# Kernel tuning notes

Hardware: AMD Instinct MI355X
Metric: run time of the kernel (lower is better)

The kernel has to match this reference:

```python
import jax, jax.numpy as jnp
import numpy as np

N = 512
C = 64
B = 1048576


def setup_inputs() -> dict:
    key = jax.random.key(0)
    k1, k2, k3, k4 = jax.random.split(key, 4)
    coords = jax.random.uniform(k1, (B, 3), dtype=jnp.float32, minval=-0.5, maxval=0.5)
    x_line = jax.random.normal(k2, (N, C), dtype=jnp.float32)
    y_line = jax.random.normal(k3, (N, C), dtype=jnp.float32)
    z_line = jax.random.normal(k4, (N, C), dtype=jnp.float32)
    grid = jnp.linspace(-0.5, 0.5, N, dtype=jnp.float32)
    return {"coords": coords, "x_line": x_line, "y_line": y_line, "z_line": z_line, "grid": grid}


def _interp_1d(line_feat, coord, grid):
    # line_feat: [N, C], coord: [B] in [-0.5, 0.5]
    n = line_feat.shape[0]
    pos = (coord - grid[0]) / (grid[1] - grid[0])          # [B] fractional index
    idx0 = jnp.clip(jnp.floor(pos).astype(jnp.int32), 0, n - 2)
    w1 = (pos - idx0.astype(pos.dtype))[:, None]            # [B, 1]
    f0 = line_feat[idx0]                                    # [B, C] gather
    f1 = line_feat[idx0 + 1]                                # [B, C] gather
    return f0 * (1.0 - w1) + f1 * w1


def reference(coords, x_line, y_line, z_line, grid):
    # mode='sum' (default): fx + fy + fz -> [B, C]
    fx = _interp_1d(x_line, coords[:, 0], grid)
    fy = _interp_1d(y_line, coords[:, 1], grid)
    fz = _interp_1d(z_line, coords[:, 2], grid)
    return fx + fy + fz
```

## Files before the change

kernel.cpp:

```cpp
#include <hip/hip_runtime.h>


typedef float f4 __attribute__((ext_vector_type(4)));

constexpr int kN  = 512;
constexpr int kC4 = 16;

__global__ __launch_bounds__(256) void triline_kernel(
    const float* __restrict__ coords,
    const f4* __restrict__ xl,
    const f4* __restrict__ yl,
    const f4* __restrict__ zl,
    const float* __restrict__ grid,
    f4* __restrict__ out,
    int total)
{
    int gid = blockIdx.x * 256 + threadIdx.x;
    if (gid >= total) return;
    int b  = gid >> 4;
    int c4 = gid & 15;

    float g0     = grid[0];
    float inv_dg = 1.0f / (grid[1] - g0);

    float cx = coords[3 * b + 0];
    float cy = coords[3 * b + 1];
    float cz = coords[3 * b + 2];

    float px = (cx - g0) * inv_dg;
    float py = (cy - g0) * inv_dg;
    float pz = (cz - g0) * inv_dg;

    int ix = min(max((int)floorf(px), 0), kN - 2);
    int iy = min(max((int)floorf(py), 0), kN - 2);
    int iz = min(max((int)floorf(pz), 0), kN - 2);

    float wx = px - (float)ix;
    float wy = py - (float)iy;
    float wz = pz - (float)iz;

    f4 x0 = xl[ix * kC4 + c4];
    f4 x1 = xl[ix * kC4 + kC4 + c4];
    f4 y0 = yl[iy * kC4 + c4];
    f4 y1 = yl[iy * kC4 + kC4 + c4];
    f4 z0 = zl[iz * kC4 + c4];
    f4 z1 = zl[iz * kC4 + kC4 + c4];

    f4 r = x0 + (x1 - x0) * wx;
    r    = r + y0 + (y1 - y0) * wy;
    r    = r + z0 + (z1 - z0) * wz;

    __builtin_nontemporal_store(r, &out[gid]);
}

extern "C" void kernel_launch(void* const* d_in, const int* in_sizes, int n_in,
                              void* d_out, int out_size, void* d_ws, size_t ws_size,
                              hipStream_t stream) {
    const float* coords = (const float*)d_in[0];
    const f4*    xl     = (const f4*)d_in[1];
    const f4*    yl     = (const f4*)d_in[2];
    const f4*    zl     = (const f4*)d_in[3];
    const float* grid   = (const float*)d_in[4];
    f4*          out    = (f4*)d_out;

    int B      = in_sizes[0] / 3;
    int total  = B * kC4;
    int blocks = (total + 255) / 256;

    triline_kernel<<<blocks, 256, 0, stream>>>(coords, xl, yl, zl, grid, out, total);
}
```

Before: 332.9 us.

## Stage channel-group slices of line tables in LDS as bf16 with persistent blocks

```diff
diff --git a/kernel.cpp b/kernel.cpp
--- a/kernel.cpp
+++ b/kernel.cpp
@@ -2,55 +2,110 @@
 
 
 typedef float f4 __attribute__((ext_vector_type(4)));
+typedef unsigned short u16;
+typedef u16 us4 __attribute__((ext_vector_type(4)));
 
-constexpr int kN  = 512;
-constexpr int kC4 = 16;
+constexpr int kN        = 512;
+constexpr int kC4       = 16;
+constexpr int kGroups   = 4;
+constexpr int kStride   = 20;
+constexpr int kParts    = 128;
+constexpr int kThreads  = 1024;
 
-__global__ __launch_bounds__(256) void triline_kernel(
+__device__ __forceinline__ u16 f32_to_bf16_rn(float f) {
+    unsigned int u = __builtin_bit_cast(unsigned int, f);
+    unsigned int r = (u + 0x7FFFu + ((u >> 16) & 1u)) >> 16;
+    return (u16)r;
+}
+__device__ __forceinline__ float bf16_to_f32(u16 h) {
+    unsigned int u = ((unsigned int)h) << 16;
+    return __builtin_bit_cast(float, u);
+}
+__device__ __forceinline__ f4 us4_to_f4(us4 h) {
+    f4 r;
+    r.x = bf16_to_f32(h.x); r.y = bf16_to_f32(h.y);
+    r.z = bf16_to_f32(h.z); r.w = bf16_to_f32(h.w);
+    return r;
+}
+
+__global__ __launch_bounds__(kThreads) void triline_kernel(
     const float* __restrict__ coords,
     const f4* __restrict__ xl,
     const f4* __restrict__ yl,
     const f4* __restrict__ zl,
     const float* __restrict__ grid,
     f4* __restrict__ out,
-    int total)
+    int B)
 {
-    int gid = blockIdx.x * 256 + threadIdx.x;
-    if (gid >= total) return;
-    int b  = gid >> 4;
-    int c4 = gid & 15;
+    __shared__ u16 s_tab[3 * kN * kStride];
+
+    const int tid   = threadIdx.x;
+    const int g     = blockIdx.x & (kGroups - 1);
+    const int part  = blockIdx.x >> 2;
+    const int pts   = B / kParts;
+    const int pbase = part * pts;
+
+    for (int s = tid; s < 3 * kN * 4; s += kThreads) {
+        int t  = s >> 11;
+        int rq = s & 2047;
+        int r  = rq >> 2;
+        int q  = rq & 3;
+        const f4* tp = (t == 0) ? xl : ((t == 1) ? yl : zl);
+        f4 v = tp[r * kC4 + g * 4 + q];
+        us4 h;
+        h.x = f32_to_bf16_rn(v.x); h.y = f32_to_bf16_rn(v.y);
+        h.z = f32_to_bf16_rn(v.z); h.w = f32_to_bf16_rn(v.w);
+        *(us4*)&s_tab[t * (kN * kStride) + r * kStride + q * 4] = h;
+    }
 
     float g0     = grid[0];
     float inv_dg = 1.0f / (grid[1] - g0);
 
-    float cx = coords[3 * b + 0];
-    float cy = coords[3 * b + 1];
-    float cz = coords[3 * b + 2];
+    __syncthreads();
 
-    float px = (cx - g0) * inv_dg;
-    float py = (cy - g0) * inv_dg;
-    float pz = (cz - g0) * inv_dg;
+    const u16* sx = &s_tab[0];
+    const u16* sy = &s_tab[kN * kStride];
+    const u16* sz = &s_tab[2 * kN * kStride];
 
-    int ix = min(max((int)floorf(px), 0), kN - 2);
-    int iy = min(max((int)floorf(py), 0), kN - 2);
-    int iz = min(max((int)floorf(pz), 0), kN - 2);
+    const int items = pts * 4;
+    for (int i = tid; i < items; i += kThreads) {
+        int p = pbase + (i >> 2);
+        int c = i & 3;
+        if (p >= B) break;
 
-    float wx = px - (float)ix;
-    float wy = py - (float)iy;
-    float wz = pz - (float)iz;
+        float cx = coords[3 * p + 0];
+        float cy = coords[3 * p + 1];
+        float cz = coords[3 * p + 2];
 
-    f4 x0 = xl[ix * kC4 + c4];
-    f4 x1 = xl[ix * kC4 + kC4 + c4];
-    f4 y0 = yl[iy * kC4 + c4];
-    f4 y1 = yl[iy * kC4 + kC4 + c4];
-    f4 z0 = zl[iz * kC4 + c4];
-    f4 z1 = zl[iz * kC4 + kC4 + c4];
+        float px = (cx - g0) * inv_dg;
+        float py = (cy - g0) * inv_dg;
+        float pz = (cz - g0) * inv_dg;
 
-    f4 r = x0 + (x1 - x0) * wx;
-    r    = r + y0 + (y1 - y0) * wy;
-    r    = r + z0 + (z1 - z0) * wz;
+        int ix = min(max((int)floorf(px), 0), kN - 2);
+        int iy = min(max((int)floorf(py), 0), kN - 2);
+        int iz = min(max((int)floorf(pz), 0), kN - 2);
 
-    __builtin_nontemporal_store(r, &out[gid]);
+        float wx = px - (float)ix;
+        float wy = py - (float)iy;
+        float wz = pz - (float)iz;
+
+        const u16* ax = sx + ix * kStride + c * 4;
+        const u16* ay = sy + iy * kStride + c * 4;
+        const u16* az = sz + iz * kStride + c * 4;
+
+        f4 x0 = us4_to_f4(*(const us4*)ax);
+        f4 x1 = us4_to_f4(*(const us4*)(ax + kStride));
+        f4 y0 = us4_to_f4(*(const us4*)ay);
+        f4 y1 = us4_to_f4(*(const us4*)(ay + kStride));
+        f4 z0 = us4_to_f4(*(const us4*)az);
+        f4 z1 = us4_to_f4(*(const us4*)(az + kStride));
+
+        f4 r = x0 + (x1 - x0) * wx;
+        r    = r + y0 + (y1 - y0) * wy;
+        r    = r + z0 + (z1 - z0) * wz;
+
+        out[p * kC4 + g * 4 + c] = r;
+    }
 }
 
 extern "C" void kernel_launch(void* const* d_in, const int* in_sizes, int n_in,
@@ -63,9 +118,8 @@
     const float* grid   = (const float*)d_in[4];
     f4*          out    = (f4*)d_out;
 
-    int B      = in_sizes[0] / 3;
-    int total  = B * kC4;
-    int blocks = (total + 255) / 256;
+    int B = in_sizes[0] / 3;
 
-    triline_kernel<<<blocks, 256, 0, stream>>>(coords, xl, yl, zl, grid, out, total);
+    dim3 grid_dim(kGroups * kParts);
+    triline_kernel<<<grid_dim, kThreads, 0, stream>>>(coords, xl, yl, zl, grid, out, B);
 }
```

Result: slower. 362.3 us (+8.8%).
